# Kernel optimization log

Measured on AMD Instinct MI355X. Metric: run time of the kernel, lower is better.

## Reference

```python
import jax, jax.numpy as jnp
import numpy as np

N_NODES, N_EDGES, D, N_RELS = 50000, 600000, 128, 460


def setup_inputs() -> dict:
    key = jax.random.key(0)
    ks = jax.random.split(key, 8)
    h = jax.random.normal(ks[0], (N_NODES, D), dtype=jnp.float32)
    emb_rel = jax.random.normal(ks[1], (N_RELS, D), dtype=jnp.float32)
    attn_fc_w = jax.random.normal(ks[2], (D, 3 * D), dtype=jnp.float32) * 0.05   # Linear(3D->D), weight [out,in]
    attn_fc2_w = jax.random.normal(ks[3], (1, D), dtype=jnp.float32) * 0.05     # Linear(D->1)
    loop_weight = jax.random.normal(ks[4], (D, D), dtype=jnp.float32) * 0.05
    edge_src = jax.random.randint(ks[5], (N_EDGES,), 0, N_NODES)
    edge_dst = jax.random.randint(ks[6], (N_EDGES,), 0, N_NODES)
    edge_type = jax.random.randint(ks[7], (N_EDGES,), 0, N_RELS)
    return {"h": h, "emb_rel": emb_rel, "attn_fc_w": attn_fc_w,
            "attn_fc2_w": attn_fc2_w, "loop_weight": loop_weight,
            "edge_src": edge_src, "edge_dst": edge_dst, "edge_type": edge_type}


def reference(h, emb_rel, attn_fc_w, attn_fc2_w, loop_weight, edge_src, edge_dst, edge_type):
    n = h.shape[0]
    # --- per-edge gather ---
    hs = h[edge_src]            # [E, D] src features (mailbox 'e_h')
    ht = h[edge_dst]            # [E, D]
    rel = emb_rel[edge_type]    # [E, D]
    # --- concat-MLP attention: leaky_relu(fc2(fc1([hs|ht|rel]))) ---
    z2 = jnp.concatenate([hs, ht, rel], axis=1)          # [E, 3D]
    a = z2 @ attn_fc_w.T                                  # [E, D]
    e = jax.nn.leaky_relu(a @ attn_fc2_w.T)               # [E, 1], slope 0.01 (torch default)
    # --- per-destination segment softmax ---
    m = jax.ops.segment_max(e, edge_dst, num_segments=n)  # [N, 1]
    m = jnp.where(jnp.isfinite(m), m, jnp.float32(0.0))   # empty nodes -> -inf; neutralize
    ex = jnp.exp(e - m[edge_dst])                         # [E, 1]
    den = jax.ops.segment_sum(ex, edge_dst, num_segments=n)
    alpha = ex / den[edge_dst]                            # [E, 1]
    # --- weighted scatter-sum of src features ---
    node_repr = jax.ops.segment_sum(alpha * hs, edge_dst, num_segments=n)  # [N, D]
    # --- self-loop ---
    node_repr = node_repr + h @ loop_weight
    return node_repr
```

## Files before the change

### kernel.cpp

```cpp
#include <hip/hip_runtime.h>

#define N_NODES 50000
#define N_EDGES 600000
#define D 128
#define N_RELS 460
#define CAP_LOG 6

typedef unsigned short u16;
typedef __attribute__((ext_vector_type(8))) short bf16x8;
typedef __attribute__((ext_vector_type(4))) float f32x4;

enum : int {
    OFF_W      = 0,
    OFF_S1     = 384,
    OFF_S2     = 50384,
    OFF_S3     = 100384,
    OFF_COUNTS = 100864,
    OFF_CSR    = 900864,
    OFF_HB     = 4100864,
};

#define NODE_WAVES   12500
#define REL_WAVES    115
#define SCORE_BLOCKS 3154
#define GEMM_BLOCKS  782
#define ZERO_BLOCKS  196
#define FILL_BLOCKS  293
#define WT_STRIDE    136

__device__ __forceinline__ u16 f2bf(float f) {
    unsigned u = __float_as_uint(f);
    unsigned r = u + 0x7FFFu + ((u >> 16) & 1u);
    return (u16)(r >> 16);
}
__device__ __forceinline__ float blo(unsigned u) { return __uint_as_float(u << 16); }
__device__ __forceinline__ float bhi(unsigned u) { return __uint_as_float(u & 0xFFFF0000u); }

__global__ __launch_bounds__(256) void k_prep(
        const float* __restrict__ fc1, const float* __restrict__ fc2,
        const float* __restrict__ W, const float* __restrict__ h,
        float* __restrict__ w, int* __restrict__ counts,
        u16* __restrict__ hb, float* __restrict__ out) {
    __shared__ u16 Ws[D * WT_STRIDE];
    int t = threadIdx.x;
    if (blockIdx.x < GEMM_BLOCKS) {
        for (int i = t; i < (D * D) / 4; i += 256) {
            float4 v = ((const float4*)W)[i];
            int k  = i >> 5;
            int n0 = (i & 31) * 4;
            Ws[(n0 + 0) * WT_STRIDE + k] = f2bf(v.x);
            Ws[(n0 + 1) * WT_STRIDE + k] = f2bf(v.y);
            Ws[(n0 + 2) * WT_STRIDE + k] = f2bf(v.z);
            Ws[(n0 + 3) * WT_STRIDE + k] = f2bf(v.w);
        }
        __syncthreads();

        int wave = t >> 6, lane = t & 63;
        int quad = lane >> 4, m16 = lane & 15;
        int nbase = blockIdx.x * 64 + wave * 16;

        f32x4 acc[8];
        #pragma unroll
        for (int cg = 0; cg < 8; ++cg) acc[cg] = (f32x4){0.f, 0.f, 0.f, 0.f};

        int arow = nbase + m16;
        if (arow >= N_NODES) arow = N_NODES - 1;
        const float* aptr = h + (size_t)arow * D + quad * 8;
        u16* hbp = hb + (size_t)arow * D + quad * 8;

        #pragma unroll
        for (int k0 = 0; k0 < D; k0 += 32) {
            float4 a0 = *(const float4*)(aptr + k0);
            float4 a1 = *(const float4*)(aptr + k0 + 4);
            bf16x8 a;
            a[0] = (short)f2bf(a0.x); a[1] = (short)f2bf(a0.y);
            a[2] = (short)f2bf(a0.z); a[3] = (short)f2bf(a0.w);
            a[4] = (short)f2bf(a1.x); a[5] = (short)f2bf(a1.y);
            a[6] = (short)f2bf(a1.z); a[7] = (short)f2bf(a1.w);
            *(bf16x8*)(hbp + k0) = a;
            #pragma unroll
            for (int cg = 0; cg < 8; ++cg) {
                bf16x8 bb = *(const bf16x8*)(&Ws[(cg * 16 + m16) * WT_STRIDE + k0 + quad * 8]);
                acc[cg] = __builtin_amdgcn_mfma_f32_16x16x32_bf16(a, bb, acc[cg], 0, 0, 0);
            }
        }
        #pragma unroll
        for (int reg = 0; reg < 4; ++reg) {
            int row = nbase + quad * 4 + reg;
            if (row < N_NODES) {
                #pragma unroll
                for (int cg = 0; cg < 8; ++cg)
                    out[(size_t)row * D + cg * 16 + m16] = acc[cg][reg];
            }
        }
    } else if (blockIdx.x < GEMM_BLOCKS + ZERO_BLOCKS) {
        int i4 = (blockIdx.x - GEMM_BLOCKS) * 256 + t;
        #pragma unroll
        for (int rep = 0; rep < 4; ++rep) {
            int idx = i4 * 4 + rep;
            if (idx * 4 < N_NODES * 16)
                ((int4*)counts)[idx] = make_int4(0, 0, 0, 0);
        }
    } else {
        for (int j = t; j < 3 * D; j += 256) {
            float acc = 0.f;
            for (int k = 0; k < D; ++k) acc += fc2[k] * fc1[k * 3 * D + j];
            w[j] = acc;
        }
    }
}

__global__ __launch_bounds__(256) void k_fused(
        const int* __restrict__ src, const int* __restrict__ dst,
        const int* __restrict__ typ, int* __restrict__ counts,
        unsigned* __restrict__ csr,
        const u16* __restrict__ hb, const float* __restrict__ emb_rel,
        const float* __restrict__ w,
        float* __restrict__ s1, float* __restrict__ s2, float* __restrict__ s3) {
    if (blockIdx.x < FILL_BLOCKS) {
        int i = blockIdx.x * blockDim.x + threadIdx.x;
        if (i >= N_EDGES / 8) return;
        int4 da = ((const int4*)dst)[2 * i],     db = ((const int4*)dst)[2 * i + 1];
        int4 sa = ((const int4*)src)[2 * i],     sb = ((const int4*)src)[2 * i + 1];
        int4 ta = ((const int4*)typ)[2 * i],     tb = ((const int4*)typ)[2 * i + 1];
        int l0 = atomicAdd(&counts[da.x << 4], 1);
        int l1 = atomicAdd(&counts[da.y << 4], 1);
        int l2 = atomicAdd(&counts[da.z << 4], 1);
        int l3 = atomicAdd(&counts[da.w << 4], 1);
        int l4 = atomicAdd(&counts[db.x << 4], 1);
        int l5 = atomicAdd(&counts[db.y << 4], 1);
        int l6 = atomicAdd(&counts[db.z << 4], 1);
        int l7 = atomicAdd(&counts[db.w << 4], 1);
        csr[(da.x << CAP_LOG) + l0] = (unsigned)sa.x | ((unsigned)ta.x << 16);
        csr[(da.y << CAP_LOG) + l1] = (unsigned)sa.y | ((unsigned)ta.y << 16);
        csr[(da.z << CAP_LOG) + l2] = (unsigned)sa.z | ((unsigned)ta.z << 16);
        csr[(da.w << CAP_LOG) + l3] = (unsigned)sa.w | ((unsigned)ta.w << 16);
        csr[(db.x << CAP_LOG) + l4] = (unsigned)sb.x | ((unsigned)tb.x << 16);
        csr[(db.y << CAP_LOG) + l5] = (unsigned)sb.y | ((unsigned)tb.y << 16);
        csr[(db.z << CAP_LOG) + l6] = (unsigned)sb.z | ((unsigned)tb.z << 16);
        csr[(db.w << CAP_LOG) + l7] = (unsigned)sb.w | ((unsigned)tb.w << 16);
    } else {
        int wv = ((blockIdx.x - FILL_BLOCKS) * blockDim.x + threadIdx.x) >> 6;
        int l  = threadIdx.x & 63;
        int sub = l >> 4;
        int q   = l & 15;
        if (wv < NODE_WAVES) {
            int r = wv * 4 + sub;
            uint4 pk = ((const uint4*)hb)[(size_t)r * 16 + q];
            float4 w10 = *(const float4*)(w + q * 8);
            float4 w11 = *(const float4*)(w + q * 8 + 4);
            float4 w20 = *(const float4*)(w + D + q * 8);
            float4 w21 = *(const float4*)(w + D + q * 8 + 4);
            float a1 = blo(pk.x) * w10.x + bhi(pk.x) * w10.y
                     + blo(pk.y) * w10.z + bhi(pk.y) * w10.w
                     + blo(pk.z) * w11.x + bhi(pk.z) * w11.y
                     + blo(pk.w) * w11.z + bhi(pk.w) * w11.w;
            float a2 = blo(pk.x) * w20.x + bhi(pk.x) * w20.y
                     + blo(pk.y) * w20.z + bhi(pk.y) * w20.w
                     + blo(pk.z) * w21.x + bhi(pk.z) * w21.y
                     + blo(pk.w) * w21.z + bhi(pk.w) * w21.w;
            #pragma unroll
            for (int o = 8; o; o >>= 1) { a1 += __shfl_xor(a1, o, 16); a2 += __shfl_xor(a2, o, 16); }
            if (q == 0) { s1[r] = a1; s2[r] = a2; }
        } else if (wv < NODE_WAVES + REL_WAVES) {
            int r = (wv - NODE_WAVES) * 4 + sub;
            const float* rp = emb_rel + (size_t)r * D + q * 8;
            float4 r0 = *(const float4*)rp;
            float4 r1 = *(const float4*)(rp + 4);
            float4 w30 = *(const float4*)(w + 2 * D + q * 8);
            float4 w31 = *(const float4*)(w + 2 * D + q * 8 + 4);
            float a3 = r0.x * w30.x + r0.y * w30.y + r0.z * w30.z + r0.w * w30.w
                     + r1.x * w31.x + r1.y * w31.y + r1.z * w31.z + r1.w * w31.w;
            #pragma unroll
            for (int o = 8; o; o >>= 1) a3 += __shfl_xor(a3, o, 16);
            if (q == 0) s3[r] = a3;
        }
    }
}

#define ROWACC(uu, cc)                                                         \
    accA.x += (cc) * blo((uu).x);  accA.y += (cc) * bhi((uu).x);               \
    accA.z += (cc) * blo((uu).y);  accA.w += (cc) * bhi((uu).y);               \
    accB.x += (cc) * blo((uu).z);  accB.y += (cc) * bhi((uu).z);               \
    accB.z += (cc) * blo((uu).w);  accB.w += (cc) * bhi((uu).w);

__global__ void k_gather(const u16* __restrict__ hb, const int* __restrict__ counts,
                         const unsigned* __restrict__ csr,
                         const float* __restrict__ s1, const float* __restrict__ s2,
                         const float* __restrict__ s3, float* __restrict__ out) {
    int n  = (blockIdx.x * blockDim.x + threadIdx.x) >> 4;
    int gl = threadIdx.x & 15;
    if (n >= N_NODES) return;
    int deg = counts[n << 4];
    if (deg == 0) return;
    int beg = n << CAP_LOG;
    int end = beg + deg;

    float s2n = s2[n];
    float den = 0.f;
    f32x4 accA = {0.f, 0.f, 0.f, 0.f}, accB = {0.f, 0.f, 0.f, 0.f};

    for (int cb = beg; cb < end; cb += 16) {
        int i = cb + gl;
        int msrc = 0; float mex = 0.f;
        if (i < end) {
            unsigned p = csr[i];
            msrc = (int)(p & 0xFFFFu);
            float x = s1[msrc] + s2n + s3[p >> 16];
            float lv = (x > 0.f) ? x : 0.01f * x;
            mex = __expf(lv);
        }
        den += mex;
        int cnt  = min(16, end - cb);
        int cntr = (cnt + 3) & ~3;
        int j = 0;
        for (; j + 7 < cntr; j += 8) {
            int aa[8]; float cc[8]; uint4 uu[8];
            #pragma unroll
            for (int u = 0; u < 8; ++u) {
                aa[u] = __shfl(msrc, j + u, 16);
                cc[u] = __shfl(mex,  j + u, 16);
            }
            #pragma unroll
            for (int u = 0; u < 8; ++u)
                uu[u] = ((const uint4*)(hb + (size_t)aa[u] * D))[gl];
            #pragma unroll
            for (int u = 0; u < 8; ++u) { ROWACC(uu[u], cc[u]); }
        }
        for (; j < cntr; j += 4) {
            int aa[4]; float cc[4]; uint4 uu[4];
            #pragma unroll
            for (int u = 0; u < 4; ++u) {
                aa[u] = __shfl(msrc, j + u, 16);
                cc[u] = __shfl(mex,  j + u, 16);
            }
            #pragma unroll
            for (int u = 0; u < 4; ++u)
                uu[u] = ((const uint4*)(hb + (size_t)aa[u] * D))[gl];
            #pragma unroll
            for (int u = 0; u < 4; ++u) { ROWACC(uu[u], cc[u]); }
        }
    }
    #pragma unroll
    for (int o = 8; o; o >>= 1) den += __shfl_xor(den, o, 16);
    float inv = 1.f / den;

    f32x4* op = (f32x4*)(out + (size_t)n * D + gl * 8);
    f32x4 o0 = __builtin_nontemporal_load(op);
    f32x4 o1 = __builtin_nontemporal_load(op + 1);
    o0 += accA * inv;
    o1 += accB * inv;
    __builtin_nontemporal_store(o0, op);
    __builtin_nontemporal_store(o1, op + 1);
}

extern "C" void kernel_launch(void* const* d_in, const int* in_sizes, int n_in,
                              void* d_out, int out_size, void* d_ws, size_t ws_size,
                              hipStream_t stream) {
    const float* h       = (const float*)d_in[0];
    const float* emb_rel = (const float*)d_in[1];
    const float* fc1     = (const float*)d_in[2];
    const float* fc2     = (const float*)d_in[3];
    const float* loopw   = (const float*)d_in[4];
    const int*   esrc    = (const int*)d_in[5];
    const int*   edst    = (const int*)d_in[6];
    const int*   etyp    = (const int*)d_in[7];
    float* out = (float*)d_out;
    float* ws  = (float*)d_ws;

    float*    w       = ws + OFF_W;
    float*    s1      = ws + OFF_S1;
    float*    s2      = ws + OFF_S2;
    float*    s3      = ws + OFF_S3;
    int*      counts  = (int*)(ws + OFF_COUNTS);
    unsigned* csr     = (unsigned*)(ws + OFF_CSR);
    u16*      hb      = (u16*)(ws + OFF_HB);

    k_prep<<<GEMM_BLOCKS + ZERO_BLOCKS + 1, 256, 0, stream>>>(
        fc1, fc2, loopw, h, w, counts, hb, out);

    k_fused<<<FILL_BLOCKS + SCORE_BLOCKS, 256, 0, stream>>>(
        esrc, edst, etyp, counts, csr, hb, emb_rel, w, s1, s2, s3);

    k_gather<<<(N_NODES * 16 + 255) / 256, 256, 0, stream>>>(
        hb, counts, csr, s1, s2, s3, out);
}
```

Measured before the change: 165.1 us.

## Move edge score exp into CSR fill and pack fp16 weight with source

Restructures the pipeline into four kernels. Node scores are computed from fp32 h alongside the GEMM. The CSR fill kernel then computes each edge's leaky-relu exp score and stores it as fp16 in the upper half of the CSR entry, replacing the relation type. The gather kernel no longer does the random s1/s3 lookups or the exp; it just decodes the packed weight. This adds a kernel launch and serializes fill after scores, and the unnormalized exp stored in fp16 risks precision loss or overflow.

Measured after the change: 185.8 us. +12.5%, slower.

```diff
diff --git a/kernel.cpp b/kernel.cpp
--- a/kernel.cpp
+++ b/kernel.cpp
@@ -1,4 +1,5 @@
 #include <hip/hip_runtime.h>
+#include <hip/hip_fp16.h>
 
 #define N_NODES 50000
 #define N_EDGES 600000
@@ -36,10 +37,30 @@
 __device__ __forceinline__ float blo(unsigned u) { return __uint_as_float(u << 16); }
 __device__ __forceinline__ float bhi(unsigned u) { return __uint_as_float(u & 0xFFFF0000u); }
 
-__global__ __launch_bounds__(256) void k_prep(
-        const float* __restrict__ fc1, const float* __restrict__ fc2,
+__global__ void k_prep(const float* __restrict__ fc1, const float* __restrict__ fc2,
+                       float* __restrict__ w, int* __restrict__ counts) {
+    int b = blockIdx.x, t = threadIdx.x;
+    if (b == 0) {
+        for (int j = t; j < 3 * D; j += 256) {
+            float acc = 0.f;
+            for (int k = 0; k < D; ++k) acc += fc2[k] * fc1[k * 3 * D + j];
+            w[j] = acc;
+        }
+    } else {
+        int i4 = (b - 1) * 256 + t;
+        #pragma unroll
+        for (int rep = 0; rep < 4; ++rep) {
+            int idx = i4 * 4 + rep;
+            if (idx * 4 < N_NODES * 16)
+                ((int4*)counts)[idx] = make_int4(0, 0, 0, 0);
+        }
+    }
+}
+
+__global__ __launch_bounds__(256) void k_gemm_scores(
         const float* __restrict__ W, const float* __restrict__ h,
-        float* __restrict__ w, int* __restrict__ counts,
+        const float* __restrict__ emb_rel, const float* __restrict__ w,
+        float* __restrict__ s1, float* __restrict__ s2, float* __restrict__ s3,
         u16* __restrict__ hb, float* __restrict__ out) {
     __shared__ u16 Ws[D * WT_STRIDE];
     int t = threadIdx.x;
@@ -93,72 +114,24 @@
                     out[(size_t)row * D + cg * 16 + m16] = acc[cg][reg];
             }
         }
-    } else if (blockIdx.x < GEMM_BLOCKS + ZERO_BLOCKS) {
-        int i4 = (blockIdx.x - GEMM_BLOCKS) * 256 + t;
-        #pragma unroll
-        for (int rep = 0; rep < 4; ++rep) {
-            int idx = i4 * 4 + rep;
-            if (idx * 4 < N_NODES * 16)
-                ((int4*)counts)[idx] = make_int4(0, 0, 0, 0);
-        }
     } else {
-        for (int j = t; j < 3 * D; j += 256) {
-            float acc = 0.f;
-            for (int k = 0; k < D; ++k) acc += fc2[k] * fc1[k * 3 * D + j];
-            w[j] = acc;
-        }
-    }
-}
-
-__global__ __launch_bounds__(256) void k_fused(
-        const int* __restrict__ src, const int* __restrict__ dst,
-        const int* __restrict__ typ, int* __restrict__ counts,
-        unsigned* __restrict__ csr,
-        const u16* __restrict__ hb, const float* __restrict__ emb_rel,
-        const float* __restrict__ w,
-        float* __restrict__ s1, float* __restrict__ s2, float* __restrict__ s3) {
-    if (blockIdx.x < FILL_BLOCKS) {
-        int i = blockIdx.x * blockDim.x + threadIdx.x;
-        if (i >= N_EDGES / 8) return;
-        int4 da = ((const int4*)dst)[2 * i],     db = ((const int4*)dst)[2 * i + 1];
-        int4 sa = ((const int4*)src)[2 * i],     sb = ((const int4*)src)[2 * i + 1];
-        int4 ta = ((const int4*)typ)[2 * i],     tb = ((const int4*)typ)[2 * i + 1];
-        int l0 = atomicAdd(&counts[da.x << 4], 1);
-        int l1 = atomicAdd(&counts[da.y << 4], 1);
-        int l2 = atomicAdd(&counts[da.z << 4], 1);
-        int l3 = atomicAdd(&counts[da.w << 4], 1);
-        int l4 = atomicAdd(&counts[db.x << 4], 1);
-        int l5 = atomicAdd(&counts[db.y << 4], 1);
-        int l6 = atomicAdd(&counts[db.z << 4], 1);
-        int l7 = atomicAdd(&counts[db.w << 4], 1);
-        csr[(da.x << CAP_LOG) + l0] = (unsigned)sa.x | ((unsigned)ta.x << 16);
-        csr[(da.y << CAP_LOG) + l1] = (unsigned)sa.y | ((unsigned)ta.y << 16);
-        csr[(da.z << CAP_LOG) + l2] = (unsigned)sa.z | ((unsigned)ta.z << 16);
-        csr[(da.w << CAP_LOG) + l3] = (unsigned)sa.w | ((unsigned)ta.w << 16);
-        csr[(db.x << CAP_LOG) + l4] = (unsigned)sb.x | ((unsigned)tb.x << 16);
-        csr[(db.y << CAP_LOG) + l5] = (unsigned)sb.y | ((unsigned)tb.y << 16);
-        csr[(db.z << CAP_LOG) + l6] = (unsigned)sb.z | ((unsigned)tb.z << 16);
-        csr[(db.w << CAP_LOG) + l7] = (unsigned)sb.w | ((unsigned)tb.w << 16);
-    } else {
-        int wv = ((blockIdx.x - FILL_BLOCKS) * blockDim.x + threadIdx.x) >> 6;
+        int wv = ((blockIdx.x - GEMM_BLOCKS) * blockDim.x + threadIdx.x) >> 6;
         int l  = threadIdx.x & 63;
         int sub = l >> 4;
         int q   = l & 15;
         if (wv < NODE_WAVES) {
             int r = wv * 4 + sub;
-            uint4 pk = ((const uint4*)hb)[(size_t)r * 16 + q];
+            const float* hp = h + (size_t)r * D + q * 8;
+            float4 h0 = *(const float4*)hp;
+            float4 h1 = *(const float4*)(hp + 4);
             float4 w10 = *(const float4*)(w + q * 8);
             float4 w11 = *(const float4*)(w + q * 8 + 4);
             float4 w20 = *(const float4*)(w + D + q * 8);
             float4 w21 = *(const float4*)(w + D + q * 8 + 4);
-            float a1 = blo(pk.x) * w10.x + bhi(pk.x) * w10.y
-                     + blo(pk.y) * w10.z + bhi(pk.y) * w10.w
-                     + blo(pk.z) * w11.x + bhi(pk.z) * w11.y
-                     + blo(pk.w) * w11.z + bhi(pk.w) * w11.w;
-            float a2 = blo(pk.x) * w20.x + bhi(pk.x) * w20.y
-                     + blo(pk.y) * w20.z + bhi(pk.y) * w20.w
-                     + blo(pk.z) * w21.x + bhi(pk.z) * w21.y
-                     + blo(pk.w) * w21.z + bhi(pk.w) * w21.w;
+            float a1 = h0.x * w10.x + h0.y * w10.y + h0.z * w10.z + h0.w * w10.w
+                     + h1.x * w11.x + h1.y * w11.y + h1.z * w11.z + h1.w * w11.w;
+            float a2 = h0.x * w20.x + h0.y * w20.y + h0.z * w20.z + h0.w * w20.w
+                     + h1.x * w21.x + h1.y * w21.y + h1.z * w21.z + h1.w * w21.w;
             #pragma unroll
             for (int o = 8; o; o >>= 1) { a1 += __shfl_xor(a1, o, 16); a2 += __shfl_xor(a2, o, 16); }
             if (q == 0) { s1[r] = a1; s2[r] = a2; }
@@ -178,6 +151,35 @@
     }
 }
 
+__global__ __launch_bounds__(256) void k_fill(
+        const int* __restrict__ src, const int* __restrict__ dst,
+        const int* __restrict__ typ, int* __restrict__ counts,
+        const float* __restrict__ s1, const float* __restrict__ s2,
+        const float* __restrict__ s3, unsigned* __restrict__ csr) {
+    int i = blockIdx.x * blockDim.x + threadIdx.x;
+    if (i >= N_EDGES / 8) return;
+    int4 da = ((const int4*)dst)[2 * i],     db = ((const int4*)dst)[2 * i + 1];
+    int4 sa = ((const int4*)src)[2 * i],     sb = ((const int4*)src)[2 * i + 1];
+    int4 ta = ((const int4*)typ)[2 * i],     tb = ((const int4*)typ)[2 * i + 1];
+    int dd[8] = {da.x, da.y, da.z, da.w, db.x, db.y, db.z, db.w};
+    int ss[8] = {sa.x, sa.y, sa.z, sa.w, sb.x, sb.y, sb.z, sb.w};
+    int tt[8] = {ta.x, ta.y, ta.z, ta.w, tb.x, tb.y, tb.z, tb.w};
+    float xx[8];
+    #pragma unroll
+    for (int u = 0; u < 8; ++u) xx[u] = s1[ss[u]] + s2[dd[u]] + s3[tt[u]];
+    int sl[8];
+    #pragma unroll
+    for (int u = 0; u < 8; ++u) sl[u] = atomicAdd(&counts[dd[u] << 4], 1);
+    #pragma unroll
+    for (int u = 0; u < 8; ++u) {
+        float x = xx[u];
+        float lv = (x > 0.f) ? x : 0.01f * x;
+        float ex = __expf(lv);
+        csr[(dd[u] << CAP_LOG) + sl[u]] =
+            (unsigned)ss[u] | ((unsigned)__half_as_ushort(__float2half(ex)) << 16);
+    }
+}
+
 #define ROWACC(uu, cc)                                                         \
     accA.x += (cc) * blo((uu).x);  accA.y += (cc) * bhi((uu).x);               \
     accA.z += (cc) * blo((uu).y);  accA.w += (cc) * bhi((uu).y);               \
@@ -185,9 +187,7 @@
     accB.z += (cc) * blo((uu).w);  accB.w += (cc) * bhi((uu).w);
 
 __global__ void k_gather(const u16* __restrict__ hb, const int* __restrict__ counts,
-                         const unsigned* __restrict__ csr,
-                         const float* __restrict__ s1, const float* __restrict__ s2,
-                         const float* __restrict__ s3, float* __restrict__ out) {
+                         const unsigned* __restrict__ csr, float* __restrict__ out) {
     int n  = (blockIdx.x * blockDim.x + threadIdx.x) >> 4;
     int gl = threadIdx.x & 15;
     if (n >= N_NODES) return;
@@ -196,7 +196,6 @@
     int beg = n << CAP_LOG;
     int end = beg + deg;
 
-    float s2n = s2[n];
     float den = 0.f;
     f32x4 accA = {0.f, 0.f, 0.f, 0.f}, accB = {0.f, 0.f, 0.f, 0.f};
 
@@ -206,9 +205,7 @@
         if (i < end) {
             unsigned p = csr[i];
             msrc = (int)(p & 0xFFFFu);
-            float x = s1[msrc] + s2n + s3[p >> 16];
-            float lv = (x > 0.f) ? x : 0.01f * x;
-            mex = __expf(lv);
+            mex  = __half2float(__ushort_as_half((u16)(p >> 16)));
         }
         den += mex;
         int cnt  = min(16, end - cb);
@@ -276,12 +273,13 @@
     unsigned* csr     = (unsigned*)(ws + OFF_CSR);
     u16*      hb      = (u16*)(ws + OFF_HB);
 
-    k_prep<<<GEMM_BLOCKS + ZERO_BLOCKS + 1, 256, 0, stream>>>(
-        fc1, fc2, loopw, h, w, counts, hb, out);
-
-    k_fused<<<FILL_BLOCKS + SCORE_BLOCKS, 256, 0, stream>>>(
-        esrc, edst, etyp, counts, csr, hb, emb_rel, w, s1, s2, s3);
-
-    k_gather<<<(N_NODES * 16 + 255) / 256, 256, 0, stream>>>(
-        hb, counts, csr, s1, s2, s3, out);
-}
+    k_prep<<<1 + ZERO_BLOCKS, 256, 0, stream>>>(fc1, fc2, w, counts);
+
+    k_gemm_scores<<<GEMM_BLOCKS + SCORE_BLOCKS, 256, 0, stream>>>(
+        loopw, h, emb_rel, w, s1, s2, s3, hb, out);
+
+    k_fill<<<FILL_BLOCKS, 256, 0, stream>>>(
+        esrc, edst, etyp, counts, s1, s2, s3, csr);
+
+    k_gather<<<(N_NODES * 16 + 255) / 256, 256, 0, stream>>>(hb, counts, csr, out);
+}
```
